# Kernel optimization log

Measured on AMD Instinct MI355X. Metric: run time of the kernel, lower is better.

## Reference

```python
import jax, jax.numpy as jnp
import numpy as np

B, N, D, H = 16, 256, 512, 8
DK = D // H          # 64
DIM_G = 64           # trigonometric geometry embedding dim
WAVE_LEN = 1000.0


def box_relational_embedding(boxes):
    # boxes: [B, N, 4] = (x_min, y_min, x_max, y_max)
    x_min, y_min, x_max, y_max = jnp.split(boxes, 4, axis=-1)  # each [B,N,1]
    cx = ((x_min + x_max) * 0.5)[..., 0]   # [B,N]
    cy = ((y_min + y_max) * 0.5)[..., 0]
    w = (x_max - x_min + 1.0)[..., 0]
    h = (y_max - y_min + 1.0)[..., 0]
    # pairwise deltas, normalized by the *row* box size (as in the torch code)
    dx = jnp.log(jnp.clip(jnp.abs((cx[:, :, None] - cx[:, None, :]) / w[:, :, None]), 1e-3))
    dy = jnp.log(jnp.clip(jnp.abs((cy[:, :, None] - cy[:, None, :]) / h[:, :, None]), 1e-3))
    dw = jnp.log(w[:, :, None] / w[:, None, :])
    dh = jnp.log(h[:, :, None] / h[:, None, :])
    pos = jnp.stack([dx, dy, dw, dh], axis=-1)  # [B,N,N,4]
    # trig embedding: freq per (dim_g/8) channels
    feat_range = jnp.arange(DIM_G // 8, dtype=pos.dtype) / (DIM_G / 8.0)
    dim_mat = 1.0 / jnp.power(WAVE_LEN, feat_range)               # [8]
    mul = (100.0 * pos)[..., None] * dim_mat                      # [B,N,N,4,8]
    mul = mul.reshape(mul.shape[:3] + (-1,))                      # [B,N,N,32]
    return jnp.concatenate([jnp.sin(mul), jnp.cos(mul)], axis=-1)  # [B,N,N,64]


def setup_inputs() -> dict:
    key = jax.random.key(0)
    ks = jax.random.split(key, 16)
    inp = {
        'input_query': jax.random.normal(ks[0], (B, N, D), jnp.float32),
        'input_key': jax.random.normal(ks[1], (B, N, D), jnp.float32),
        'input_value': jax.random.normal(ks[2], (B, N, D), jnp.float32),
    }
    # valid boxes: x_max > x_min, y_max > y_min
    xm = jax.random.uniform(ks[3], (B, N, 1)) * 800.0
    ym = jax.random.uniform(ks[4], (B, N, 1)) * 800.0
    bw = jax.random.uniform(ks[5], (B, N, 1)) * 120.0 + 5.0
    bh = jax.random.uniform(ks[6], (B, N, 1)) * 120.0 + 5.0
    inp['input_box'] = jnp.concatenate([xm, ym, xm + bw, ym + bh], axis=-1)
    s = 1.0 / np.sqrt(D)
    inp['Wq'] = jax.random.normal(ks[7], (D, D), jnp.float32) * s
    inp['bq'] = jnp.zeros((D,), jnp.float32)
    inp['Wk'] = jax.random.normal(ks[8], (D, D), jnp.float32) * s
    inp['bk'] = jnp.zeros((D,), jnp.float32)
    inp['Wv'] = jax.random.normal(ks[9], (D, D), jnp.float32) * s
    inp['bv'] = jnp.zeros((D,), jnp.float32)
    inp['Wo'] = jax.random.normal(ks[10], (D, D), jnp.float32) * s
    inp['bo'] = jnp.zeros((D,), jnp.float32)
    inp['Wg'] = jax.random.normal(ks[11], (H, DIM_G), jnp.float32) * (1.0 / np.sqrt(DIM_G))
    inp['bg'] = jnp.zeros((H,), jnp.float32)
    return inp


def reference(input_query, input_key, input_value, input_box,
              Wq, bq, Wk, bk, Wv, bv, Wo, bo, Wg, bg):
    nb = input_query.shape[0]
    geo = box_relational_embedding(input_box)                     # [B,N,N,64]
    wg = jax.nn.relu(jnp.einsum('bijg,hg->bhij', geo, Wg) + bg[None, :, None, None])
    def proj(x, W, b):
        return (x @ W + b).reshape(nb, -1, H, DK).transpose(0, 2, 1, 3)  # [B,H,N,dk]
    q = proj(input_query, Wq, bq)
    k = proj(input_key, Wk, bk)
    v = proj(input_value, Wv, bv)
    scores = jnp.einsum('bhid,bhjd->bhij', q, k) / np.sqrt(DK)    # [B,H,N,N]
    w_mn = jax.nn.softmax(jnp.log(jnp.clip(wg, 1e-6)) + scores, axis=-1)
    out = jnp.einsum('bhij,bhjd->bhid', w_mn, v)                  # [B,H,N,dk]
    out = out.transpose(0, 2, 1, 3).reshape(nb, -1, H * DK)       # [B,N,D]
    return out @ Wo + bo
```

## Files before the change

kernel.cpp:

```cpp
#include <hip/hip_runtime.h>
#include <hip/hip_bf16.h>

#define B_ 16
#define N_ 256
#define D_ 512
#define H_ 8
#define DK_ 64

typedef unsigned short u16;
typedef __attribute__((ext_vector_type(8))) short bf16x8;
typedef __attribute__((ext_vector_type(4))) float f32x4;

__device__ __forceinline__ float bf2f(u16 u) {
    union { unsigned int i; float f; } v;
    v.i = ((unsigned int)u) << 16;
    return v.f;
}
__device__ __forceinline__ u16 f2bf(float f) {
    union { float f; unsigned int i; } v;
    v.f = f;
    unsigned int x = v.i;
    unsigned int r = (x >> 16) & 1u;
    x += 0x7fffu + r;
    return (u16)(x >> 16);
}

__global__ __launch_bounds__(256) void k_prep(const float* __restrict__ X0,
                                              const float* __restrict__ X1,
                                              const float* __restrict__ X2,
                                              u16* __restrict__ Xb,
                                              const float* __restrict__ W0,
                                              const float* __restrict__ W1,
                                              const float* __restrict__ W2,
                                              const float* __restrict__ W3,
                                              u16* __restrict__ Wt) {
    const int bid = blockIdx.x;
    const int tid = threadIdx.x;
    if (bid < 3072) {
        int z = bid >> 10, x = bid & 1023;
        const float* X = (z == 0) ? X0 : (z == 1) ? X1 : X2;
        u16* dst = Xb + (size_t)z * 2097152;
        int base = (x * 256 + tid) * 8;
        float4 a = *(const float4*)&X[base];
        float4 b = *(const float4*)&X[base + 4];
        ushort4 oa, ob;
        oa.x = f2bf(a.x); oa.y = f2bf(a.y); oa.z = f2bf(a.z); oa.w = f2bf(a.w);
        ob.x = f2bf(b.x); ob.y = f2bf(b.y); ob.z = f2bf(b.z); ob.w = f2bf(b.w);
        *(ushort4*)&dst[base] = oa;
        *(ushort4*)&dst[base + 4] = ob;
    } else {
        int t = bid - 3072;
        int z = t >> 8, yb = (t >> 4) & 15, xb = t & 15;
        const float* W = (z == 0) ? W0 : (z == 1) ? W1 : (z == 2) ? W2 : W3;
        u16* dst = Wt + (size_t)z * 262144;
        __shared__ float tt[32][33];
        const int kb = yb * 32, nb = xb * 32;
#pragma unroll
        for (int r = 0; r < 4; ++r) {
            int p = r * 256 + tid;
            tt[p >> 5][p & 31] = W[(size_t)(kb + (p >> 5)) * 512 + nb + (p & 31)];
        }
        __syncthreads();
#pragma unroll
        for (int r = 0; r < 4; ++r) {
            int p = r * 256 + tid;
            dst[(size_t)(nb + (p >> 5)) * 512 + kb + (p & 31)] = f2bf(tt[p & 31][p >> 5]);
        }
    }
}

#define GEMM_CORE_DB(Ab, Wt)                                                  \
    __shared__ u16 As[2][64][72];                                             \
    __shared__ u16 Bs[2][64][72];                                             \
    const int tid = threadIdx.x;                                              \
    const int n0 = blockIdx.x * 64, m0 = blockIdx.y * 64;                     \
    const int wid = tid >> 6, lane = tid & 63;                                \
    const int wm = (wid & 1) * 32, wn = (wid >> 1) * 32;                      \
    const int lr = lane & 15, lk8 = (lane >> 4) * 8;                          \
    f32x4 acc[2][2];                                                          \
    _Pragma("unroll") for (int mi = 0; mi < 2; ++mi)                          \
        _Pragma("unroll") for (int ni = 0; ni < 2; ++ni)                      \
            acc[mi][ni] = (f32x4){0.f, 0.f, 0.f, 0.f};                        \
    ushort4 ra[4], rb[4];                                                     \
    _Pragma("unroll") for (int r = 0; r < 4; ++r) {                           \
        int p = r * 256 + tid, row = p >> 4, c4 = (p & 15) * 4;               \
        ra[r] = *(const ushort4*)&Ab[(size_t)(m0 + row) * 512 + c4];          \
        rb[r] = *(const ushort4*)&Wt[(size_t)(n0 + row) * 512 + c4];          \
    }                                                                         \
    _Pragma("unroll") for (int r = 0; r < 4; ++r) {                           \
        int p = r * 256 + tid, row = p >> 4, c4 = (p & 15) * 4;               \
        *(ushort4*)&As[0][row][c4] = ra[r];                                   \
        *(ushort4*)&Bs[0][row][c4] = rb[r];                                   \
    }                                                                         \
    __syncthreads();                                                          \
    for (int it = 0; it < 8; ++it) {                                          \
        const int cur = it & 1;                                               \
        if (it < 7) {                                                         \
            int k0n = (it + 1) * 64;                                          \
            _Pragma("unroll") for (int r = 0; r < 4; ++r) {                   \
                int p = r * 256 + tid, row = p >> 4, c4 = (p & 15) * 4;       \
                ra[r] = *(const ushort4*)&Ab[(size_t)(m0 + row) * 512 + k0n + c4]; \
                rb[r] = *(const ushort4*)&Wt[(size_t)(n0 + row) * 512 + k0n + c4]; \
            }                                                                 \
        }                                                                     \
        _Pragma("unroll") for (int ks = 0; ks < 64; ks += 32) {               \
            bf16x8 af[2], bfx[2];                                             \
            _Pragma("unroll") for (int mi = 0; mi < 2; ++mi)                  \
                af[mi] = *(const bf16x8*)&As[cur][wm + mi * 16 + lr][ks + lk8]; \
            _Pragma("unroll") for (int ni = 0; ni < 2; ++ni)                  \
                bfx[ni] = *(const bf16x8*)&Bs[cur][wn + ni * 16 + lr][ks + lk8]; \
            _Pragma("unroll") for (int mi = 0; mi < 2; ++mi)                  \
                _Pragma("unroll") for (int ni = 0; ni < 2; ++ni)              \
                    acc[mi][ni] = __builtin_amdgcn_mfma_f32_16x16x32_bf16(    \
                        af[mi], bfx[ni], acc[mi][ni], 0, 0, 0);               \
        }                                                                     \
        if (it < 7) {                                                         \
            _Pragma("unroll") for (int r = 0; r < 4; ++r) {                   \
                int p = r * 256 + tid, row = p >> 4, c4 = (p & 15) * 4;       \
                *(ushort4*)&As[1 - cur][row][c4] = ra[r];                     \
                *(ushort4*)&Bs[1 - cur][row][c4] = rb[r];                     \
            }                                                                 \
            __syncthreads();                                                  \
        }                                                                     \
    }

__global__ __launch_bounds__(256) void k_gemm_qkv(const u16* __restrict__ Xb,
                                                  const u16* __restrict__ Wtb,
                                                  const float* __restrict__ bq,
                                                  const float* __restrict__ bk,
                                                  const float* __restrict__ bv,
                                                  u16* __restrict__ qkv) {
    const int z = blockIdx.z;
    const u16* Ab = Xb + (size_t)z * 2097152;
    const u16* Wt = Wtb + (size_t)z * 262144;
    const float* bias = (z == 0) ? bq : (z == 1) ? bk : bv;
    u16* outp = qkv + (size_t)z * 2097152;
    GEMM_CORE_DB(Ab, Wt)
#pragma unroll
    for (int mi = 0; mi < 2; ++mi)
#pragma unroll
        for (int ni = 0; ni < 2; ++ni) {
            int col = n0 + wn + ni * 16 + lr;
            float bb = bias[col];
            int h = col >> 6, dk = col & 63;
#pragma unroll
            for (int reg = 0; reg < 4; ++reg) {
                int m = m0 + wm + mi * 16 + (lane >> 4) * 4 + reg;
                int b = m >> 8, rr = m & 255;
                outp[(((size_t)(b * H_ + h) * N_) + rr) * DK_ + dk] =
                    f2bf(acc[mi][ni][reg] + bb);
            }
        }
}

__global__ __launch_bounds__(256) void k_gemm_out(const u16* __restrict__ Ab,
                                                  const u16* __restrict__ Wt,
                                                  const float* __restrict__ bias,
                                                  float* __restrict__ outp) {
    GEMM_CORE_DB(Ab, Wt)
#pragma unroll
    for (int mi = 0; mi < 2; ++mi)
#pragma unroll
        for (int ni = 0; ni < 2; ++ni) {
            int col = n0 + wn + ni * 16 + lr;
            float bb = bias[col];
#pragma unroll
            for (int reg = 0; reg < 4; ++reg) {
                int m = m0 + wm + mi * 16 + (lane >> 4) * 4 + reg;
                outp[(size_t)m * 512 + col] = acc[mi][ni][reg] + bb;
            }
        }
}

__global__ __launch_bounds__(256) void k_geo(const float* __restrict__ box,
                                             const float* __restrict__ Wg,
                                             const float* __restrict__ bg,
                                             u16* __restrict__ Sg) {
    __shared__ float sWg[8][64];
    __shared__ float sbg[8];
    const int tid = threadIdx.x;
    if (tid < 8) sbg[tid] = bg[tid];
    { int e = tid; sWg[e >> 6][e & 63] = Wg[e];
      e = tid + 256; sWg[e >> 6][e & 63] = Wg[e]; }
    const int bi = blockIdx.x, b = bi >> 8;
    float4 bxi = *(const float4*)&box[(size_t)bi * 4];
    float4 bxj = *(const float4*)&box[(size_t)(b * N_ + tid) * 4];
    __syncthreads();
    float cxi = (bxi.x + bxi.z) * 0.5f, cyi = (bxi.y + bxi.w) * 0.5f;
    float wi = bxi.z - bxi.x + 1.0f, hi = bxi.w - bxi.y + 1.0f;
    float cxj = (bxj.x + bxj.z) * 0.5f, cyj = (bxj.y + bxj.w) * 0.5f;
    float wj = bxj.z - bxj.x + 1.0f, hj = bxj.w - bxj.y + 1.0f;
    float pos[4];
    pos[0] = __logf(fmaxf(fabsf((cxi - cxj) / wi), 1e-3f));
    pos[1] = __logf(fmaxf(fabsf((cyi - cyj) / hi), 1e-3f));
    pos[2] = __logf(wi / wj);
    pos[3] = __logf(hi / hj);
    const float dm[8] = {1.0f, 0.42169650342858224f, 0.1778279410038923f,
                         0.07498942093324559f, 0.03162277660168379f,
                         0.013335214321633241f, 0.005623413251903491f,
                         0.0023713737056616554f};
    float acc[8];
#pragma unroll
    for (int h = 0; h < 8; ++h) acc[h] = sbg[h];
#pragma unroll
    for (int t = 0; t < 4; ++t) {
        float base = 100.0f * pos[t];
#pragma unroll
        for (int f = 0; f < 8; ++f) {
            float sn, cs;
            __sincosf(base * dm[f], &sn, &cs);
            int idx = t * 8 + f;
#pragma unroll
            for (int h = 0; h < 8; ++h)
                acc[h] += sWg[h][idx] * sn + sWg[h][idx + 32] * cs;
        }
    }
    const int i = bi & 255;
#pragma unroll
    for (int h = 0; h < 8; ++h)
        Sg[(((size_t)(b * H_ + h) * N_) + i) * N_ + tid] =
            f2bf(__logf(fmaxf(acc[h], 1e-6f)));
}

__global__ __launch_bounds__(256) void k_attn(const u16* __restrict__ qh,
                                              const u16* __restrict__ kh,
                                              const u16* __restrict__ vh,
                                              const u16* __restrict__ Sg,
                                              u16* __restrict__ attnb) {
    __shared__ __align__(16) unsigned char smem[58368];
    u16* sQ = (u16*)smem;
    u16* sK = (u16*)(smem + 4608);
    float* sS = (float*)(smem + 4608);
    u16* sVt = (u16*)(smem + 4608);
    u16* sP = (u16*)(smem + 41472);

    const int tid = threadIdx.x;
    const int i0 = blockIdx.x * 32;
    const int bh = blockIdx.y;
    const int b = bh >> 3, h = bh & 7;
    const int wid = tid >> 6, lane = tid & 63;
    const int lr = lane & 15, lk8 = (lane >> 4) * 8, quad4 = (lane >> 4) * 4;

#pragma unroll
    for (int r = 0; r < 2; ++r) {
        int p = r * 256 + tid, i = p >> 4, d0 = (p & 15) * 4;
        *(ushort4*)&sQ[i * 72 + d0] =
            *(const ushort4*)&qh[((size_t)bh * N_ + i0 + i) * DK_ + d0];
    }
#pragma unroll
    for (int r = 0; r < 16; ++r) {
        int p = r * 256 + tid, j = p >> 4, d0 = (p & 15) * 4;
        *(ushort4*)&sK[j * 72 + d0] =
            *(const ushort4*)&kh[((size_t)bh * N_ + j) * DK_ + d0];
    }
    __syncthreads();

    f32x4 acc[2][4];
#pragma unroll
    for (int mi = 0; mi < 2; ++mi)
#pragma unroll
        for (int ni = 0; ni < 4; ++ni) acc[mi][ni] = (f32x4){0.f, 0.f, 0.f, 0.f};
    const int wn = wid * 64;
#pragma unroll
    for (int ks = 0; ks < 64; ks += 32) {
        bf16x8 af[2], bfx[4];
#pragma unroll
        for (int mi = 0; mi < 2; ++mi)
            af[mi] = *(const bf16x8*)&sQ[(mi * 16 + lr) * 72 + ks + lk8];
#pragma unroll
        for (int ni = 0; ni < 4; ++ni)
            bfx[ni] = *(const bf16x8*)&sK[(wn + ni * 16 + lr) * 72 + ks + lk8];
#pragma unroll
        for (int mi = 0; mi < 2; ++mi)
#pragma unroll
            for (int ni = 0; ni < 4; ++ni)
                acc[mi][ni] = __builtin_amdgcn_mfma_f32_16x16x32_bf16(
                    af[mi], bfx[ni], acc[mi][ni], 0, 0, 0);
    }
    __syncthreads();

#pragma unroll
    for (int mi = 0; mi < 2; ++mi)
#pragma unroll
        for (int ni = 0; ni < 4; ++ni) {
            int col = wn + ni * 16 + lr;
#pragma unroll
            for (int reg = 0; reg < 4; ++reg) {
                int row = mi * 16 + quad4 + reg;
                float bias = bf2f(Sg[(((size_t)bh * N_) + i0 + row) * N_ + col]);
                sS[row * 260 + col] = acc[mi][ni][reg] * 0.125f + bias;
            }
        }
    __syncthreads();

#pragma unroll
    for (int rr = 0; rr < 8; ++rr) {
        int row = rr * 4 + wid;
        float4 x = *(float4*)&sS[row * 260 + lane * 4];
        float mx = fmaxf(fmaxf(x.x, x.y), fmaxf(x.z, x.w));
#pragma unroll
        for (int off = 32; off >= 1; off >>= 1) mx = fmaxf(mx, __shfl_xor(mx, off, 64));
        float e0 = __expf(x.x - mx), e1 = __expf(x.y - mx);
        float e2 = __expf(x.z - mx), e3 = __expf(x.w - mx);
        float s = e0 + e1 + e2 + e3;
#pragma unroll
        for (int off = 32; off >= 1; off >>= 1) s += __shfl_xor(s, off, 64);
        float inv = 1.0f / s;
        ushort4 p4;
        p4.x = f2bf(e0 * inv); p4.y = f2bf(e1 * inv);
        p4.z = f2bf(e2 * inv); p4.w = f2bf(e3 * inv);
        *(ushort4*)&sP[row * 264 + lane * 4] = p4;
    }
    __syncthreads();

#pragma unroll
    for (int r = 0; r < 16; ++r) {
        int p = r * 256 + tid, j = p >> 4, d0 = (p & 15) * 4;
        ushort4 vv = *(const ushort4*)&vh[((size_t)bh * N_ + j) * DK_ + d0];
        sVt[(d0 + 0) * 264 + j] = vv.x;
        sVt[(d0 + 1) * 264 + j] = vv.y;
        sVt[(d0 + 2) * 264 + j] = vv.z;
        sVt[(d0 + 3) * 264 + j] = vv.w;
    }
    __syncthreads();

    f32x4 acc2[2];
    acc2[0] = (f32x4){0.f, 0.f, 0.f, 0.f};
    acc2[1] = (f32x4){0.f, 0.f, 0.f, 0.f};
    const int wd = wid * 16;
#pragma unroll
    for (int ks8 = 0; ks8 < 8; ++ks8) {
        int k0 = ks8 * 32;
        bf16x8 bfx = *(const bf16x8*)&sVt[(wd + lr) * 264 + k0 + lk8];
#pragma unroll
        for (int mi = 0; mi < 2; ++mi) {
            bf16x8 af = *(const bf16x8*)&sP[(mi * 16 + lr) * 264 + k0 + lk8];
            acc2[mi] = __builtin_amdgcn_mfma_f32_16x16x32_bf16(af, bfx, acc2[mi], 0, 0, 0);
        }
    }
#pragma unroll
    for (int mi = 0; mi < 2; ++mi)
#pragma unroll
        for (int reg = 0; reg < 4; ++reg) {
            int row = mi * 16 + quad4 + reg;
            attnb[((size_t)(b * N_ + i0 + row)) * D_ + h * 64 + wd + lr] =
                f2bf(acc2[mi][reg]);
        }
}

extern "C" void kernel_launch(void* const* d_in, const int* in_sizes, int n_in,
                              void* d_out, int out_size, void* d_ws, size_t ws_size,
                              hipStream_t stream) {
    const float* Xq = (const float*)d_in[0];
    const float* Xk = (const float*)d_in[1];
    const float* Xv = (const float*)d_in[2];
    const float* box = (const float*)d_in[3];
    const float* Wq = (const float*)d_in[4];
    const float* bq = (const float*)d_in[5];
    const float* Wk = (const float*)d_in[6];
    const float* bk = (const float*)d_in[7];
    const float* Wv = (const float*)d_in[8];
    const float* bv = (const float*)d_in[9];
    const float* Wo = (const float*)d_in[10];
    const float* bo = (const float*)d_in[11];
    const float* Wg = (const float*)d_in[12];
    const float* bg = (const float*)d_in[13];
    float* out = (float*)d_out;

    u16* ws16 = (u16*)d_ws;
    u16* qkv = ws16;
    u16* qh = qkv;
    u16* kh = qkv + 2097152;
    u16* vh = qkv + 4194304;
    u16* Sg = ws16 + 6291456;
    u16* Xb = ws16 + 6291456;
    u16* attnb = ws16 + 14680064;
    u16* Wt = ws16 + 16777216;

    dim3 blk(256);
    k_prep<<<dim3(4096), blk, 0, stream>>>(Xq, Xk, Xv, Xb, Wq, Wk, Wv, Wo, Wt);
    k_gemm_qkv<<<dim3(8, 64, 3), blk, 0, stream>>>(Xb, Wt, bq, bk, bv, qkv);
    k_geo<<<dim3(B_ * N_), blk, 0, stream>>>(box, Wg, bg, Sg);
    k_attn<<<dim3(8, 128), blk, 0, stream>>>(qh, kh, vh, Sg, attnb);
    k_gemm_out<<<dim3(8, 64), blk, 0, stream>>>(attnb, Wt + 3 * 262144, bo, out);
}
```

Baseline: 184.8 us.

## Fuse input bf16 conversion into QKV GEMM, pre-transpose V, register-resident softmax

Drops the separate activation fp32-to-bf16 pass by converting inputs inside the QKV GEMM load path. The GEMM epilogue now stages results through shared memory for coalesced stores, folds the 1/sqrt(dk) scale into Q, and writes V already transposed. The attention kernel keeps scores in MFMA registers, does the softmax with cross-wave reductions through small shared buffers, and loads transposed V in two halves to cut shared-memory use. This removes an HBM round trip and the strided V transpose, at the cost of more registers and extra barriers in the attention kernel.

```diff
diff --git a/kernel.cpp b/kernel.cpp
--- a/kernel.cpp
+++ b/kernel.cpp
@@ -25,139 +25,229 @@
     return (u16)(x >> 16);
 }
 
-__global__ __launch_bounds__(256) void k_prep(const float* __restrict__ X0,
-                                              const float* __restrict__ X1,
-                                              const float* __restrict__ X2,
-                                              u16* __restrict__ Xb,
-                                              const float* __restrict__ W0,
-                                              const float* __restrict__ W1,
-                                              const float* __restrict__ W2,
-                                              const float* __restrict__ W3,
-                                              u16* __restrict__ Wt) {
-    const int bid = blockIdx.x;
+__global__ __launch_bounds__(256) void k_wtrans(const float* __restrict__ W0,
+                                                const float* __restrict__ W1,
+                                                const float* __restrict__ W2,
+                                                const float* __restrict__ W3,
+                                                u16* __restrict__ Wt) {
+    const float* W = (blockIdx.z == 0) ? W0 : (blockIdx.z == 1) ? W1
+                     : (blockIdx.z == 2) ? W2 : W3;
+    u16* dst = Wt + (size_t)blockIdx.z * 262144;
+    __shared__ float t[32][33];
     const int tid = threadIdx.x;
-    if (bid < 3072) {
-        int z = bid >> 10, x = bid & 1023;
-        const float* X = (z == 0) ? X0 : (z == 1) ? X1 : X2;
-        u16* dst = Xb + (size_t)z * 2097152;
-        int base = (x * 256 + tid) * 8;
-        float4 a = *(const float4*)&X[base];
-        float4 b = *(const float4*)&X[base + 4];
-        ushort4 oa, ob;
-        oa.x = f2bf(a.x); oa.y = f2bf(a.y); oa.z = f2bf(a.z); oa.w = f2bf(a.w);
-        ob.x = f2bf(b.x); ob.y = f2bf(b.y); ob.z = f2bf(b.z); ob.w = f2bf(b.w);
-        *(ushort4*)&dst[base] = oa;
-        *(ushort4*)&dst[base + 4] = ob;
-    } else {
-        int t = bid - 3072;
-        int z = t >> 8, yb = (t >> 4) & 15, xb = t & 15;
-        const float* W = (z == 0) ? W0 : (z == 1) ? W1 : (z == 2) ? W2 : W3;
-        u16* dst = Wt + (size_t)z * 262144;
-        __shared__ float tt[32][33];
-        const int kb = yb * 32, nb = xb * 32;
-#pragma unroll
-        for (int r = 0; r < 4; ++r) {
-            int p = r * 256 + tid;
-            tt[p >> 5][p & 31] = W[(size_t)(kb + (p >> 5)) * 512 + nb + (p & 31)];
-        }
-        __syncthreads();
-#pragma unroll
-        for (int r = 0; r < 4; ++r) {
-            int p = r * 256 + tid;
-            dst[(size_t)(nb + (p >> 5)) * 512 + kb + (p & 31)] = f2bf(tt[p & 31][p >> 5]);
-        }
-    }
-}
-
-#define GEMM_CORE_DB(Ab, Wt)                                                  \
-    __shared__ u16 As[2][64][72];                                             \
-    __shared__ u16 Bs[2][64][72];                                             \
-    const int tid = threadIdx.x;                                              \
-    const int n0 = blockIdx.x * 64, m0 = blockIdx.y * 64;                     \
-    const int wid = tid >> 6, lane = tid & 63;                                \
-    const int wm = (wid & 1) * 32, wn = (wid >> 1) * 32;                      \
-    const int lr = lane & 15, lk8 = (lane >> 4) * 8;                          \
-    f32x4 acc[2][2];                                                          \
-    _Pragma("unroll") for (int mi = 0; mi < 2; ++mi)                          \
-        _Pragma("unroll") for (int ni = 0; ni < 2; ++ni)                      \
-            acc[mi][ni] = (f32x4){0.f, 0.f, 0.f, 0.f};                        \
-    ushort4 ra[4], rb[4];                                                     \
-    _Pragma("unroll") for (int r = 0; r < 4; ++r) {                           \
-        int p = r * 256 + tid, row = p >> 4, c4 = (p & 15) * 4;               \
-        ra[r] = *(const ushort4*)&Ab[(size_t)(m0 + row) * 512 + c4];          \
-        rb[r] = *(const ushort4*)&Wt[(size_t)(n0 + row) * 512 + c4];          \
-    }                                                                         \
-    _Pragma("unroll") for (int r = 0; r < 4; ++r) {                           \
-        int p = r * 256 + tid, row = p >> 4, c4 = (p & 15) * 4;               \
-        *(ushort4*)&As[0][row][c4] = ra[r];                                   \
-        *(ushort4*)&Bs[0][row][c4] = rb[r];                                   \
-    }                                                                         \
-    __syncthreads();                                                          \
-    for (int it = 0; it < 8; ++it) {                                          \
-        const int cur = it & 1;                                               \
-        if (it < 7) {                                                         \
-            int k0n = (it + 1) * 64;                                          \
-            _Pragma("unroll") for (int r = 0; r < 4; ++r) {                   \
-                int p = r * 256 + tid, row = p >> 4, c4 = (p & 15) * 4;       \
-                ra[r] = *(const ushort4*)&Ab[(size_t)(m0 + row) * 512 + k0n + c4]; \
-                rb[r] = *(const ushort4*)&Wt[(size_t)(n0 + row) * 512 + k0n + c4]; \
-            }                                                                 \
-        }                                                                     \
-        _Pragma("unroll") for (int ks = 0; ks < 64; ks += 32) {               \
-            bf16x8 af[2], bfx[2];                                             \
-            _Pragma("unroll") for (int mi = 0; mi < 2; ++mi)                  \
-                af[mi] = *(const bf16x8*)&As[cur][wm + mi * 16 + lr][ks + lk8]; \
-            _Pragma("unroll") for (int ni = 0; ni < 2; ++ni)                  \
-                bfx[ni] = *(const bf16x8*)&Bs[cur][wn + ni * 16 + lr][ks + lk8]; \
-            _Pragma("unroll") for (int mi = 0; mi < 2; ++mi)                  \
-                _Pragma("unroll") for (int ni = 0; ni < 2; ++ni)              \
-                    acc[mi][ni] = __builtin_amdgcn_mfma_f32_16x16x32_bf16(    \
-                        af[mi], bfx[ni], acc[mi][ni], 0, 0, 0);               \
-        }                                                                     \
-        if (it < 7) {                                                         \
-            _Pragma("unroll") for (int r = 0; r < 4; ++r) {                   \
-                int p = r * 256 + tid, row = p >> 4, c4 = (p & 15) * 4;       \
-                *(ushort4*)&As[1 - cur][row][c4] = ra[r];                     \
-                *(ushort4*)&Bs[1 - cur][row][c4] = rb[r];                     \
-            }                                                                 \
-            __syncthreads();                                                  \
-        }                                                                     \
-    }
-
-__global__ __launch_bounds__(256) void k_gemm_qkv(const u16* __restrict__ Xb,
+    const int kb = blockIdx.y * 32, nb = blockIdx.x * 32;
+#pragma unroll
+    for (int r = 0; r < 4; ++r) {
+        int p = r * 256 + tid;
+        t[p >> 5][p & 31] = W[(size_t)(kb + (p >> 5)) * 512 + nb + (p & 31)];
+    }
+    __syncthreads();
+#pragma unroll
+    for (int r = 0; r < 4; ++r) {
+        int p = r * 256 + tid;
+        dst[(size_t)(nb + (p >> 5)) * 512 + kb + (p & 31)] = f2bf(t[p & 31][p >> 5]);
+    }
+}
+
+__global__ __launch_bounds__(256) void k_gemm_qkv(const float* __restrict__ Xq,
+                                                  const float* __restrict__ Xk,
+                                                  const float* __restrict__ Xv,
                                                   const u16* __restrict__ Wtb,
                                                   const float* __restrict__ bq,
                                                   const float* __restrict__ bk,
                                                   const float* __restrict__ bv,
                                                   u16* __restrict__ qkv) {
     const int z = blockIdx.z;
-    const u16* Ab = Xb + (size_t)z * 2097152;
+    const float* A = (z == 0) ? Xq : (z == 1) ? Xk : Xv;
     const u16* Wt = Wtb + (size_t)z * 262144;
     const float* bias = (z == 0) ? bq : (z == 1) ? bk : bv;
-    u16* outp = qkv + (size_t)z * 2097152;
-    GEMM_CORE_DB(Ab, Wt)
-#pragma unroll
-    for (int mi = 0; mi < 2; ++mi)
-#pragma unroll
-        for (int ni = 0; ni < 2; ++ni) {
-            int col = n0 + wn + ni * 16 + lr;
-            float bb = bias[col];
-            int h = col >> 6, dk = col & 63;
-#pragma unroll
-            for (int reg = 0; reg < 4; ++reg) {
-                int m = m0 + wm + mi * 16 + (lane >> 4) * 4 + reg;
-                int b = m >> 8, rr = m & 255;
-                outp[(((size_t)(b * H_ + h) * N_) + rr) * DK_ + dk] =
-                    f2bf(acc[mi][ni][reg] + bb);
-            }
-        }
+    u16* dst = qkv + (size_t)z * 2097152;
+
+    __shared__ u16 As[2][64][72];
+    __shared__ u16 Bs[2][64][72];
+    const int tid = threadIdx.x;
+    const int n0 = blockIdx.x * 64, m0 = blockIdx.y * 64;
+    const int wid = tid >> 6, lane = tid & 63;
+    const int wm = (wid & 1) * 32, wn = (wid >> 1) * 32;
+    const int lr = lane & 15, lk8 = (lane >> 4) * 8, quad4 = (lane >> 4) * 4;
+
+    f32x4 acc[2][2];
+#pragma unroll
+    for (int mi = 0; mi < 2; ++mi)
+#pragma unroll
+        for (int ni = 0; ni < 2; ++ni) acc[mi][ni] = (f32x4){0.f, 0.f, 0.f, 0.f};
+
+    float4 raf[4];
+    ushort4 rb[4];
+#pragma unroll
+    for (int r = 0; r < 4; ++r) {
+        int p = r * 256 + tid, row = p >> 4, c4 = (p & 15) * 4;
+        raf[r] = *(const float4*)&A[(size_t)(m0 + row) * 512 + c4];
+        rb[r] = *(const ushort4*)&Wt[(size_t)(n0 + row) * 512 + c4];
+    }
+#pragma unroll
+    for (int r = 0; r < 4; ++r) {
+        int p = r * 256 + tid, row = p >> 4, c4 = (p & 15) * 4;
+        ushort4 ab;
+        ab.x = f2bf(raf[r].x); ab.y = f2bf(raf[r].y);
+        ab.z = f2bf(raf[r].z); ab.w = f2bf(raf[r].w);
+        *(ushort4*)&As[0][row][c4] = ab;
+        *(ushort4*)&Bs[0][row][c4] = rb[r];
+    }
+    __syncthreads();
+    for (int it = 0; it < 8; ++it) {
+        const int cur = it & 1;
+        if (it < 7) {
+            int k0n = (it + 1) * 64;
+#pragma unroll
+            for (int r = 0; r < 4; ++r) {
+                int p = r * 256 + tid, row = p >> 4, c4 = (p & 15) * 4;
+                raf[r] = *(const float4*)&A[(size_t)(m0 + row) * 512 + k0n + c4];
+                rb[r] = *(const ushort4*)&Wt[(size_t)(n0 + row) * 512 + k0n + c4];
+            }
+        }
+#pragma unroll
+        for (int ks = 0; ks < 64; ks += 32) {
+            bf16x8 af[2], bfx[2];
+#pragma unroll
+            for (int mi = 0; mi < 2; ++mi)
+                af[mi] = *(const bf16x8*)&As[cur][wm + mi * 16 + lr][ks + lk8];
+#pragma unroll
+            for (int ni = 0; ni < 2; ++ni)
+                bfx[ni] = *(const bf16x8*)&Bs[cur][wn + ni * 16 + lr][ks + lk8];
+#pragma unroll
+            for (int mi = 0; mi < 2; ++mi)
+#pragma unroll
+                for (int ni = 0; ni < 2; ++ni)
+                    acc[mi][ni] = __builtin_amdgcn_mfma_f32_16x16x32_bf16(
+                        af[mi], bfx[ni], acc[mi][ni], 0, 0, 0);
+        }
+        if (it < 7) {
+#pragma unroll
+            for (int r = 0; r < 4; ++r) {
+                int p = r * 256 + tid, row = p >> 4, c4 = (p & 15) * 4;
+                ushort4 ab;
+                ab.x = f2bf(raf[r].x); ab.y = f2bf(raf[r].y);
+                ab.z = f2bf(raf[r].z); ab.w = f2bf(raf[r].w);
+                *(ushort4*)&As[1 - cur][row][c4] = ab;
+                *(ushort4*)&Bs[1 - cur][row][c4] = rb[r];
+            }
+            __syncthreads();
+        }
+    }
+    u16* bounce = &As[0][0][0];
+    const float scale = (z == 0) ? 0.125f : 1.0f;
+    const int h = n0 >> 6, b = m0 >> 8, rrb = m0 & 255;
+    if (z == 2) {
+#pragma unroll
+        for (int mi = 0; mi < 2; ++mi)
+#pragma unroll
+            for (int ni = 0; ni < 2; ++ni) {
+                int cn = wn + ni * 16 + lr;
+                float bb = bias[n0 + cn];
+#pragma unroll
+                for (int reg = 0; reg < 4; ++reg) {
+                    int rm = wm + mi * 16 + quad4 + reg;
+                    bounce[cn * 72 + rm] = f2bf(acc[mi][ni][reg] + bb);
+                }
+            }
+        __syncthreads();
+#pragma unroll
+        for (int r = 0; r < 4; ++r) {
+            int p = r * 256 + tid, dn = p >> 4, c4 = (p & 15) * 4;
+            *(ushort4*)&dst[(((size_t)(b * H_ + h) * DK_) + dn) * N_ + rrb + c4] =
+                *(const ushort4*)&bounce[dn * 72 + c4];
+        }
+    } else {
+#pragma unroll
+        for (int mi = 0; mi < 2; ++mi)
+#pragma unroll
+            for (int ni = 0; ni < 2; ++ni) {
+                int cn = wn + ni * 16 + lr;
+                float bb = bias[n0 + cn];
+#pragma unroll
+                for (int reg = 0; reg < 4; ++reg) {
+                    int rm = wm + mi * 16 + quad4 + reg;
+                    bounce[rm * 72 + cn] = f2bf((acc[mi][ni][reg] + bb) * scale);
+                }
+            }
+        __syncthreads();
+#pragma unroll
+        for (int r = 0; r < 4; ++r) {
+            int p = r * 256 + tid, rm = p >> 4, c4 = (p & 15) * 4;
+            *(ushort4*)&dst[(((size_t)(b * H_ + h) * N_) + rrb + rm) * DK_ + c4] =
+                *(const ushort4*)&bounce[rm * 72 + c4];
+        }
+    }
 }
 
 __global__ __launch_bounds__(256) void k_gemm_out(const u16* __restrict__ Ab,
                                                   const u16* __restrict__ Wt,
                                                   const float* __restrict__ bias,
                                                   float* __restrict__ outp) {
-    GEMM_CORE_DB(Ab, Wt)
+    __shared__ u16 As[2][64][72];
+    __shared__ u16 Bs[2][64][72];
+    const int tid = threadIdx.x;
+    const int n0 = blockIdx.x * 64, m0 = blockIdx.y * 64;
+    const int wid = tid >> 6, lane = tid & 63;
+    const int wm = (wid & 1) * 32, wn = (wid >> 1) * 32;
+    const int lr = lane & 15, lk8 = (lane >> 4) * 8;
+    f32x4 acc[2][2];
+#pragma unroll
+    for (int mi = 0; mi < 2; ++mi)
+#pragma unroll
+        for (int ni = 0; ni < 2; ++ni) acc[mi][ni] = (f32x4){0.f, 0.f, 0.f, 0.f};
+    ushort4 ra[4], rb[4];
+#pragma unroll
+    for (int r = 0; r < 4; ++r) {
+        int p = r * 256 + tid, row = p >> 4, c4 = (p & 15) * 4;
+        ra[r] = *(const ushort4*)&Ab[(size_t)(m0 + row) * 512 + c4];
+        rb[r] = *(const ushort4*)&Wt[(size_t)(n0 + row) * 512 + c4];
+    }
+#pragma unroll
+    for (int r = 0; r < 4; ++r) {
+        int p = r * 256 + tid, row = p >> 4, c4 = (p & 15) * 4;
+        *(ushort4*)&As[0][row][c4] = ra[r];
+        *(ushort4*)&Bs[0][row][c4] = rb[r];
+    }
+    __syncthreads();
+    for (int it = 0; it < 8; ++it) {
+        const int cur = it & 1;
+        if (it < 7) {
+            int k0n = (it + 1) * 64;
+#pragma unroll
+            for (int r = 0; r < 4; ++r) {
+                int p = r * 256 + tid, row = p >> 4, c4 = (p & 15) * 4;
+                ra[r] = *(const ushort4*)&Ab[(size_t)(m0 + row) * 512 + k0n + c4];
+                rb[r] = *(const ushort4*)&Wt[(size_t)(n0 + row) * 512 + k0n + c4];
+            }
+        }
+#pragma unroll
+        for (int ks = 0; ks < 64; ks += 32) {
+            bf16x8 af[2], bfx[2];
+#pragma unroll
+            for (int mi = 0; mi < 2; ++mi)
+                af[mi] = *(const bf16x8*)&As[cur][wm + mi * 16 + lr][ks + lk8];
+#pragma unroll
+            for (int ni = 0; ni < 2; ++ni)
+                bfx[ni] = *(const bf16x8*)&Bs[cur][wn + ni * 16 + lr][ks + lk8];
+#pragma unroll
+            for (int mi = 0; mi < 2; ++mi)
+#pragma unroll
+                for (int ni = 0; ni < 2; ++ni)
+                    acc[mi][ni] = __builtin_amdgcn_mfma_f32_16x16x32_bf16(
+                        af[mi], bfx[ni], acc[mi][ni], 0, 0, 0);
+        }
+        if (it < 7) {
+#pragma unroll
+            for (int r = 0; r < 4; ++r) {
+                int p = r * 256 + tid, row = p >> 4, c4 = (p & 15) * 4;
+                *(ushort4*)&As[1 - cur][row][c4] = ra[r];
+                *(ushort4*)&Bs[1 - cur][row][c4] = rb[r];
+            }
+            __syncthreads();
+        }
+    }
 #pragma unroll
     for (int mi = 0; mi < 2; ++mi)
 #pragma unroll
@@ -224,15 +314,16 @@
 
 __global__ __launch_bounds__(256) void k_attn(const u16* __restrict__ qh,
                                               const u16* __restrict__ kh,
-                                              const u16* __restrict__ vh,
+                                              const u16* __restrict__ vhT,
                                               const u16* __restrict__ Sg,
                                               u16* __restrict__ attnb) {
-    __shared__ __align__(16) unsigned char smem[58368];
+    __shared__ __align__(16) unsigned char smem[40960];
     u16* sQ = (u16*)smem;
-    u16* sK = (u16*)(smem + 4608);
-    float* sS = (float*)(smem + 4608);
-    u16* sVt = (u16*)(smem + 4608);
-    u16* sP = (u16*)(smem + 41472);
+    u16* sP = (u16*)(smem + 4608);
+    u16* sK = (u16*)(smem + 21504);
+    u16* sVt = (u16*)(smem + 21504);
+    float* sRedM = (float*)(smem + 39936);
+    float* sRedS = (float*)(smem + 40448);
 
     const int tid = threadIdx.x;
     const int i0 = blockIdx.x * 32;
@@ -248,94 +339,200 @@
             *(const ushort4*)&qh[((size_t)bh * N_ + i0 + i) * DK_ + d0];
     }
 #pragma unroll
-    for (int r = 0; r < 16; ++r) {
+    for (int r = 0; r < 8; ++r) {
+        int p = r * 256 + tid, row = p >> 6, jc = (p & 63) * 4;
+        *(ushort4*)&sP[row * 264 + jc] =
+            *(const ushort4*)&Sg[(((size_t)bh * N_) + i0 + row) * N_ + jc];
+    }
+#pragma unroll
+    for (int r = 0; r < 8; ++r) {
         int p = r * 256 + tid, j = p >> 4, d0 = (p & 15) * 4;
         *(ushort4*)&sK[j * 72 + d0] =
             *(const ushort4*)&kh[((size_t)bh * N_ + j) * DK_ + d0];
     }
     __syncthreads();
 
-    f32x4 acc[2][4];
-#pragma unroll
-    for (int mi = 0; mi < 2; ++mi)
-#pragma unroll
-        for (int ni = 0; ni < 4; ++ni) acc[mi][ni] = (f32x4){0.f, 0.f, 0.f, 0.f};
-    const int wn = wid * 64;
+    ushort4 kpre[8];
+#pragma unroll
+    for (int r = 0; r < 8; ++r) {
+        int p = r * 256 + tid, j = p >> 4, d0 = (p & 15) * 4;
+        kpre[r] = *(const ushort4*)&kh[((size_t)bh * N_ + 128 + j) * DK_ + d0];
+    }
+    f32x4 acc[2][2][2];
+#pragma unroll
+    for (int c = 0; c < 2; ++c)
+#pragma unroll
+        for (int mi = 0; mi < 2; ++mi)
+#pragma unroll
+            for (int ni = 0; ni < 2; ++ni) acc[c][mi][ni] = (f32x4){0.f, 0.f, 0.f, 0.f};
 #pragma unroll
     for (int ks = 0; ks < 64; ks += 32) {
-        bf16x8 af[2], bfx[4];
+        bf16x8 af[2], bfx[2];
 #pragma unroll
         for (int mi = 0; mi < 2; ++mi)
             af[mi] = *(const bf16x8*)&sQ[(mi * 16 + lr) * 72 + ks + lk8];
 #pragma unroll
-        for (int ni = 0; ni < 4; ++ni)
-            bfx[ni] = *(const bf16x8*)&sK[(wn + ni * 16 + lr) * 72 + ks + lk8];
-#pragma unroll
-        for (int mi = 0; mi < 2; ++mi)
-#pragma unroll
-            for (int ni = 0; ni < 4; ++ni)
-                acc[mi][ni] = __builtin_amdgcn_mfma_f32_16x16x32_bf16(
-                    af[mi], bfx[ni], acc[mi][ni], 0, 0, 0);
-    }
-    __syncthreads();
-
-#pragma unroll
-    for (int mi = 0; mi < 2; ++mi)
-#pragma unroll
-        for (int ni = 0; ni < 4; ++ni) {
-            int col = wn + ni * 16 + lr;
-#pragma unroll
-            for (int reg = 0; reg < 4; ++reg) {
-                int row = mi * 16 + quad4 + reg;
-                float bias = bf2f(Sg[(((size_t)bh * N_) + i0 + row) * N_ + col]);
-                sS[row * 260 + col] = acc[mi][ni][reg] * 0.125f + bias;
-            }
-        }
-    __syncthreads();
-
-#pragma unroll
-    for (int rr = 0; rr < 8; ++rr) {
-        int row = rr * 4 + wid;
-        float4 x = *(float4*)&sS[row * 260 + lane * 4];
-        float mx = fmaxf(fmaxf(x.x, x.y), fmaxf(x.z, x.w));
-#pragma unroll
-        for (int off = 32; off >= 1; off >>= 1) mx = fmaxf(mx, __shfl_xor(mx, off, 64));
-        float e0 = __expf(x.x - mx), e1 = __expf(x.y - mx);
-        float e2 = __expf(x.z - mx), e3 = __expf(x.w - mx);
-        float s = e0 + e1 + e2 + e3;
-#pragma unroll
-        for (int off = 32; off >= 1; off >>= 1) s += __shfl_xor(s, off, 64);
-        float inv = 1.0f / s;
-        ushort4 p4;
-        p4.x = f2bf(e0 * inv); p4.y = f2bf(e1 * inv);
-        p4.z = f2bf(e2 * inv); p4.w = f2bf(e3 * inv);
-        *(ushort4*)&sP[row * 264 + lane * 4] = p4;
-    }
-    __syncthreads();
-
-#pragma unroll
-    for (int r = 0; r < 16; ++r) {
+        for (int ni = 0; ni < 2; ++ni)
+            bfx[ni] = *(const bf16x8*)&sK[(wid * 32 + ni * 16 + lr) * 72 + ks + lk8];
+#pragma unroll
+        for (int mi = 0; mi < 2; ++mi)
+#pragma unroll
+            for (int ni = 0; ni < 2; ++ni)
+                acc[0][mi][ni] = __builtin_amdgcn_mfma_f32_16x16x32_bf16(
+                    af[mi], bfx[ni], acc[0][mi][ni], 0, 0, 0);
+    }
+    __syncthreads();
+#pragma unroll
+    for (int r = 0; r < 8; ++r) {
         int p = r * 256 + tid, j = p >> 4, d0 = (p & 15) * 4;
-        ushort4 vv = *(const ushort4*)&vh[((size_t)bh * N_ + j) * DK_ + d0];
-        sVt[(d0 + 0) * 264 + j] = vv.x;
-        sVt[(d0 + 1) * 264 + j] = vv.y;
-        sVt[(d0 + 2) * 264 + j] = vv.z;
-        sVt[(d0 + 3) * 264 + j] = vv.w;
-    }
-    __syncthreads();
-
-    f32x4 acc2[2];
-    acc2[0] = (f32x4){0.f, 0.f, 0.f, 0.f};
-    acc2[1] = (f32x4){0.f, 0.f, 0.f, 0.f};
-    const int wd = wid * 16;
-#pragma unroll
-    for (int ks8 = 0; ks8 < 8; ++ks8) {
-        int k0 = ks8 * 32;
-        bf16x8 bfx = *(const bf16x8*)&sVt[(wd + lr) * 264 + k0 + lk8];
+        *(ushort4*)&sK[j * 72 + d0] = kpre[r];
+    }
+    __syncthreads();
+#pragma unroll
+    for (int ks = 0; ks < 64; ks += 32) {
+        bf16x8 af[2], bfx[2];
+#pragma unroll
+        for (int mi = 0; mi < 2; ++mi)
+            af[mi] = *(const bf16x8*)&sQ[(mi * 16 + lr) * 72 + ks + lk8];
+#pragma unroll
+        for (int ni = 0; ni < 2; ++ni)
+            bfx[ni] = *(const bf16x8*)&sK[(wid * 32 + ni * 16 + lr) * 72 + ks + lk8];
+#pragma unroll
+        for (int mi = 0; mi < 2; ++mi)
+#pragma unroll
+            for (int ni = 0; ni < 2; ++ni)
+                acc[1][mi][ni] = __builtin_amdgcn_mfma_f32_16x16x32_bf16(
+                    af[mi], bfx[ni], acc[1][mi][ni], 0, 0, 0);
+    }
+    __syncthreads();
+
+#pragma unroll
+    for (int r = 0; r < 8; ++r) {
+        int p = r * 256 + tid, d = p >> 5, jc = (p & 31) * 4;
+        *(ushort4*)&sVt[d * 136 + jc] =
+            *(const ushort4*)&vhT[(((size_t)bh * DK_) + d) * N_ + jc];
+    }
+#pragma unroll
+    for (int c = 0; c < 2; ++c)
+#pragma unroll
+        for (int mi = 0; mi < 2; ++mi)
+#pragma unroll
+            for (int ni = 0; ni < 2; ++ni) {
+                int col = c * 128 + wid * 32 + ni * 16 + lr;
+#pragma unroll
+                for (int reg = 0; reg < 4; ++reg) {
+                    int row = mi * 16 + quad4 + reg;
+                    acc[c][mi][ni][reg] += bf2f(sP[row * 264 + col]);
+                }
+            }
+    float mrow[2][4];
+#pragma unroll
+    for (int mi = 0; mi < 2; ++mi)
+#pragma unroll
+        for (int reg = 0; reg < 4; ++reg) {
+            float m = acc[0][mi][0][reg];
+            m = fmaxf(m, acc[0][mi][1][reg]);
+            m = fmaxf(m, acc[1][mi][0][reg]);
+            m = fmaxf(m, acc[1][mi][1][reg]);
+#pragma unroll
+            for (int off = 1; off <= 8; off <<= 1) m = fmaxf(m, __shfl_xor(m, off, 64));
+            mrow[mi][reg] = m;
+        }
+    if (lr == 0) {
+#pragma unroll
+        for (int mi = 0; mi < 2; ++mi)
+#pragma unroll
+            for (int reg = 0; reg < 4; ++reg)
+                sRedM[(mi * 16 + quad4 + reg) * 4 + wid] = mrow[mi][reg];
+    }
+    __syncthreads();
+    float gm[2][4], sl[2][4];
+#pragma unroll
+    for (int mi = 0; mi < 2; ++mi)
+#pragma unroll
+        for (int reg = 0; reg < 4; ++reg) {
+            float4 mm = *(const float4*)&sRedM[(mi * 16 + quad4 + reg) * 4];
+            gm[mi][reg] = fmaxf(fmaxf(mm.x, mm.y), fmaxf(mm.z, mm.w));
+            sl[mi][reg] = 0.f;
+        }
+#pragma unroll
+    for (int c = 0; c < 2; ++c)
+#pragma unroll
+        for (int mi = 0; mi < 2; ++mi)
+#pragma unroll
+            for (int ni = 0; ni < 2; ++ni)
+#pragma unroll
+                for (int reg = 0; reg < 4; ++reg) {
+                    float e = __expf(acc[c][mi][ni][reg] - gm[mi][reg]);
+                    acc[c][mi][ni][reg] = e;
+                    sl[mi][reg] += e;
+                }
+#pragma unroll
+    for (int mi = 0; mi < 2; ++mi)
+#pragma unroll
+        for (int reg = 0; reg < 4; ++reg) {
+            float s = sl[mi][reg];
+#pragma unroll
+            for (int off = 1; off <= 8; off <<= 1) s += __shfl_xor(s, off, 64);
+            sl[mi][reg] = s;
+        }
+    if (lr == 0) {
+#pragma unroll
+        for (int mi = 0; mi < 2; ++mi)
+#pragma unroll
+            for (int reg = 0; reg < 4; ++reg)
+                sRedS[(mi * 16 + quad4 + reg) * 4 + wid] = sl[mi][reg];
+    }
+    __syncthreads();
+#pragma unroll
+    for (int mi = 0; mi < 2; ++mi)
+#pragma unroll
+        for (int reg = 0; reg < 4; ++reg) {
+            float4 ss = *(const float4*)&sRedS[(mi * 16 + quad4 + reg) * 4];
+            gm[mi][reg] = 1.0f / (ss.x + ss.y + ss.z + ss.w);
+        }
+#pragma unroll
+    for (int c = 0; c < 2; ++c)
+#pragma unroll
+        for (int mi = 0; mi < 2; ++mi)
+#pragma unroll
+            for (int ni = 0; ni < 2; ++ni) {
+                int col = c * 128 + wid * 32 + ni * 16 + lr;
+#pragma unroll
+                for (int reg = 0; reg < 4; ++reg) {
+                    int row = mi * 16 + quad4 + reg;
+                    sP[row * 264 + col] = f2bf(acc[c][mi][ni][reg] * gm[mi][reg]);
+                }
+            }
+    __syncthreads();
+
+    f32x4 o[2];
+    o[0] = (f32x4){0.f, 0.f, 0.f, 0.f};
+    o[1] = (f32x4){0.f, 0.f, 0.f, 0.f};
+#pragma unroll
+    for (int k0 = 0; k0 < 128; k0 += 32) {
+        bf16x8 bfx = *(const bf16x8*)&sVt[(wid * 16 + lr) * 136 + k0 + lk8];
 #pragma unroll
         for (int mi = 0; mi < 2; ++mi) {
             bf16x8 af = *(const bf16x8*)&sP[(mi * 16 + lr) * 264 + k0 + lk8];
-            acc2[mi] = __builtin_amdgcn_mfma_f32_16x16x32_bf16(af, bfx, acc2[mi], 0, 0, 0);
+            o[mi] = __builtin_amdgcn_mfma_f32_16x16x32_bf16(af, bfx, o[mi], 0, 0, 0);
+        }
+    }
+    __syncthreads();
+#pragma unroll
+    for (int r = 0; r < 8; ++r) {
+        int p = r * 256 + tid, d = p >> 5, jc = (p & 31) * 4;
+        *(ushort4*)&sVt[d * 136 + jc] =
+            *(const ushort4*)&vhT[(((size_t)bh * DK_) + d) * N_ + 128 + jc];
+    }
+    __syncthreads();
+#pragma unroll
+    for (int k0 = 0; k0 < 128; k0 += 32) {
+        bf16x8 bfx = *(const bf16x8*)&sVt[(wid * 16 + lr) * 136 + k0 + lk8];
+#pragma unroll
+        for (int mi = 0; mi < 2; ++mi) {
+            bf16x8 af = *(const bf16x8*)&sP[(mi * 16 + lr) * 264 + 128 + k0 + lk8];
+            o[mi] = __builtin_amdgcn_mfma_f32_16x16x32_bf16(af, bfx, o[mi], 0, 0, 0);
         }
     }
 #pragma unroll
@@ -343,8 +540,8 @@
 #pragma unroll
         for (int reg = 0; reg < 4; ++reg) {
             int row = mi * 16 + quad4 + reg;
-            attnb[((size_t)(b * N_ + i0 + row)) * D_ + h * 64 + wd + lr] =
-                f2bf(acc2[mi][reg]);
+            attnb[((size_t)(b * N_ + i0 + row)) * D_ + h * 64 + wid * 16 + lr] =
+                f2bf(o[mi][reg]);
         }
 }
 
@@ -371,16 +568,15 @@
     u16* qkv = ws16;
     u16* qh = qkv;
     u16* kh = qkv + 2097152;
-    u16* vh = qkv + 4194304;
+    u16* vhT = qkv + 4194304;
     u16* Sg = ws16 + 6291456;
-    u16* Xb = ws16 + 6291456;
     u16* attnb = ws16 + 14680064;
     u16* Wt = ws16 + 16777216;
 
     dim3 blk(256);
-    k_prep<<<dim3(4096), blk, 0, stream>>>(Xq, Xk, Xv, Xb, Wq, Wk, Wv, Wo, Wt);
-    k_gemm_qkv<<<dim3(8, 64, 3), blk, 0, stream>>>(Xb, Wt, bq, bk, bv, qkv);
+    k_wtrans<<<dim3(16, 16, 4), blk, 0, stream>>>(Wq, Wk, Wv, Wo, Wt);
+    k_gemm_qkv<<<dim3(8, 64, 3), blk, 0, stream>>>(Xq, Xk, Xv, Wt, bq, bk, bv, qkv);
     k_geo<<<dim3(B_ * N_), blk, 0, stream>>>(box, Wg, bg, Sg);
-    k_attn<<<dim3(8, 128), blk, 0, stream>>>(qh, kh, vh, Sg, attnb);
+    k_attn<<<dim3(8, 128), blk, 0, stream>>>(qh, kh, vhT, Sg, attnb);
     k_gemm_out<<<dim3(8, 64), blk, 0, stream>>>(attnb, Wt + 3 * 262144, bo, out);
 }
```

After: 182.8 us. About the same (-1.1%).
